# Kernel optimization log

Hardware: AMD Instinct MI355X
Metric: run time of the kernel (lower is better)

The kernel has to match this reference:

```python
import jax, jax.numpy as jnp
import numpy as np

N = 160000          # active voxels / points
C = 128             # embed_channels
K = 27              # 3x3x3 submanifold conv kernel volume
NUM_CLUSTERS = 2048
BN_EPS = 1e-5


def setup_inputs() -> dict:
    key = jax.random.key(0)
    ks = jax.random.split(key, 16)
    s = 0.05
    inp = {
        "feat": jax.random.normal(ks[0], (N, C), jnp.float32),
        "cluster0": jax.random.randint(ks[1], (N,), 0, NUM_CLUSTERS, jnp.int32),
        "cluster1": jax.random.randint(ks[2], (N,), 0, NUM_CLUSTERS, jnp.int32),
        "cluster2": jax.random.randint(ks[3], (N,), 0, NUM_CLUSTERS, jnp.int32),
        "nbr_idx": jax.random.randint(ks[4], (N, K), 0, N, jnp.int32),
        "nbr_mask": jax.random.randint(ks[5], (N, K), 0, 2, jnp.int32) > 0,
        "lw_W": jax.random.normal(ks[6], (3, C, C), jnp.float32) * s,
        "lw_gamma": jnp.ones((3, C), jnp.float32),
        "lw_beta": jnp.zeros((3, C), jnp.float32),
        "w_W": jax.random.normal(ks[7], (3, C, C), jnp.float32) * s,
        "proj_W": jax.random.normal(ks[8], (4, C, C), jnp.float32) * s,
        "proj_gamma": jnp.ones((4, C), jnp.float32),
        "proj_beta": jnp.zeros((4, C), jnp.float32),
        "adaptive_W": jax.random.normal(ks[9], (C, 3), jnp.float32) * s,
        "fuse_W": jax.random.normal(ks[10], (2 * C, C), jnp.float32) * s,
        "fuse_gamma": jnp.ones((C,), jnp.float32),
        "fuse_beta": jnp.zeros((C,), jnp.float32),
        "conv_W": jax.random.normal(ks[11], (2, K, C, C), jnp.float32) * 0.02,
        "conv_gamma": jnp.ones((2, C), jnp.float32),
        "conv_beta": jnp.zeros((2, C), jnp.float32),
    }
    return inp


def _bn(x, gamma, beta):
    # BatchNorm1d, training mode: per-channel stats over points, biased var
    m = jnp.mean(x, axis=0)
    v = jnp.var(x, axis=0)
    return (x - m) * jax.lax.rsqrt(v + BN_EPS) * gamma + beta


def _seg_sum(x, seg):
    return jax.ops.segment_sum(x, seg, num_segments=NUM_CLUSTERS)


def _seg_mean(x, seg):
    s = _seg_sum(x, seg)
    cnt = jax.ops.segment_sum(jnp.ones((x.shape[0], 1), x.dtype), seg,
                              num_segments=NUM_CLUSTERS)
    return s / jnp.maximum(cnt, 1.0)


def _subm_conv(x, W, nbr_idx, nbr_mask):
    # submanifold 3x3x3 conv on active sites: masked gather + per-offset GEMM
    m = nbr_mask.astype(x.dtype)  # [N, K]
    out = jnp.zeros_like(x)
    for k in range(K):
        out = out + (x[nbr_idx[:, k]] * m[:, k:k + 1]) @ W[k]
    return out


def reference(feat, cluster0, cluster1, cluster2, nbr_idx, nbr_mask,
              lw_W, lw_gamma, lw_beta, w_W, proj_W, proj_gamma, proj_beta,
              adaptive_W, fuse_W, fuse_gamma, fuse_beta,
              conv_W, conv_gamma, conv_beta):
    clusters = [cluster0, cluster1, cluster2]
    feats = []
    for i, cl in enumerate(clusters):
        pw = jax.nn.relu(_bn(feat @ lw_W[i], lw_gamma[i], lw_beta[i]))
        pw = pw - _seg_mean(pw, cl)[cl]
        pw = pw @ w_W[i]
        pw = jnp.exp(pw - jnp.max(pw))                      # global max
        pw = pw / (_seg_sum(pw, cl)[cl] + 1e-6)
        pfeat = jax.nn.relu(_bn(feat @ proj_W[i], proj_gamma[i], proj_beta[i])) * pw
        pfeat = _seg_sum(pfeat, cl)[cl]
        feats.append(pfeat)

    adp = jax.nn.softmax(feat @ adaptive_W, axis=1)          # [N, 3]
    feats = jnp.stack(feats, axis=1)                         # [N, 3, C]
    fused_branch = jnp.einsum('ln,lnc->lc', adp, feats)

    f = jax.nn.relu(_bn(feat @ proj_W[3], proj_gamma[3], proj_beta[3]))
    f = jnp.concatenate([f, fused_branch], axis=1)           # [N, 2C]
    f = jax.nn.relu(_bn(f @ fuse_W, fuse_gamma, fuse_beta)) + feat

    res = f
    h = _subm_conv(f, conv_W[0], nbr_idx, nbr_mask)
    h = jax.nn.relu(_bn(h, conv_gamma[0], conv_beta[0]))
    h = _subm_conv(h, conv_W[1], nbr_idx, nbr_mask)
    h = _bn(h, conv_gamma[1], conv_beta[1])
    return jax.nn.relu(h + res)
```

## Files before the change

kernel.cpp:

```cpp
#include <hip/hip_runtime.h>
#include <stdint.h>

#define N_PTS 160000
#define C 128
#define K27 27
#define NCLU 2048
#define BN_EPS 1e-5f
#define KP 136
#define KP2 264

typedef float f32x4 __attribute__((ext_vector_type(4)));
typedef short s16x8 __attribute__((ext_vector_type(8)));

__device__ __forceinline__ float bf2f(unsigned short u){
  union { unsigned int i; float f; } v; v.i = ((unsigned int)u) << 16; return v.f;
}
__device__ __forceinline__ unsigned short f2bf(float f){
  union { float f; unsigned int i; } v; v.f = f;
  unsigned int u = v.i;
  u += 0x7FFFu + ((u >> 16) & 1u);
  return (unsigned short)(u >> 16);
}
__device__ __forceinline__ unsigned int pk(float a, float b){
  return (unsigned int)f2bf(a) | ((unsigned int)f2bf(b) << 16);
}
__device__ __forceinline__ void up2(int w, float& a, float& b){
  a = bf2f((unsigned short)(w & 0xFFFF));
  b = bf2f((unsigned short)(((unsigned int)w) >> 16));
}
__device__ __forceinline__ unsigned int encf(float f){
  union { float f; unsigned int i; } v; v.f = f;
  return ((int)v.i < 0) ? ~v.i : (v.i | 0x80000000u);
}
__device__ __forceinline__ float decf(unsigned int e){
  union { unsigned int i; float f; } v;
  v.i = ((int)e < 0) ? (e ^ 0x80000000u) : ~e;
  return v.f;
}
__device__ __forceinline__ void bn_coef(const float* st, const float* gamma, const float* beta,
                                        int c, float& sc, float& sh){
  float mean = st[c] * (1.0f / N_PTS);
  float var  = st[C + c] * (1.0f / N_PTS) - mean * mean;
  float g = gamma[c] * rsqrtf(fmaxf(var, 0.f) + BN_EPS);
  sc = g; sh = beta[c] - mean * g;
}

__global__ void k_prep_weights(const float* __restrict__ lw, const float* __restrict__ w,
                               const float* __restrict__ proj, const float* __restrict__ conv,
                               const float* __restrict__ fuse,
                               unsigned short* __restrict__ tlw, unsigned short* __restrict__ tw,
                               unsigned short* __restrict__ tproj, unsigned short* __restrict__ tconv,
                               unsigned short* __restrict__ tfuse)
{
  int z = blockIdx.x, tid = threadIdx.x;
  if (z < 64){
    const float* src; unsigned short* dst; bool swz = false;
    if (z < 3){ src = lw + z*16384; dst = tlw + z*16384; }
    else if (z < 6){ src = w + (z-3)*16384; dst = tw + (z-3)*16384; }
    else if (z < 10){ src = proj + (z-6)*16384; dst = tproj + (z-6)*16384; }
    else { src = conv + (z-10)*16384; dst = tconv + (z-10)*16384; swz = true; }
    for (int i = tid; i < 16384; i += 256){
      int n = i >> 7, k = i & 127;
      int pos = swz ? (n*128 + (((k >> 3) ^ (n & 7)) << 3) + (k & 7)) : i;
      dst[pos] = f2bf(src[k*128 + n]);
    }
  } else {
    for (int i = tid; i < 32768; i += 256){
      int n = i >> 8, k = i & 255;
      tfuse[i] = f2bf(fuse[k*128 + n]);
    }
  }
}

__global__ void k_detect_mask(const unsigned int* __restrict__ mw, int* __restrict__ mmode)
{
  __shared__ int flag;
  if (threadIdx.x == 0) flag = 0;
  __syncthreads();
  for (int i = threadIdx.x; i < 4096; i += 256)
    if (mw[i] > 1u) flag = 1;
  __syncthreads();
  if (threadIdx.x == 0) *mmode = flag;
}

__global__ void k_hist(const int* __restrict__ c0, const int* __restrict__ c1,
                       const int* __restrict__ c2, int* __restrict__ hist)
{
  int idx = blockIdx.x*blockDim.x + threadIdx.x;
  int stride = gridDim.x*blockDim.x;
  for (; idx < 3*N_PTS; idx += stride){
    int j = idx / N_PTS, r = idx - j*N_PTS;
    const int* cp = (j==0)?c0:((j==1)?c1:c2);
    atomicAdd(&hist[j*NCLU + cp[r]], 1);
  }
}

__global__ void k_prefix(const int* __restrict__ hist, int* __restrict__ starts,
                         int* __restrict__ cursor)
{
  int j = blockIdx.x, tid = threadIdx.x;
  __shared__ int buf[NCLU];
  __shared__ int csum[256];
  for (int i = tid; i < NCLU; i += 256) buf[i] = hist[j*NCLU + i];
  __syncthreads();
  int s = 0;
  #pragma unroll
  for (int k = 0; k < 8; k++) s += buf[tid*8 + k];
  csum[tid] = s;
  __syncthreads();
  if (tid == 0){
    int run = 0;
    for (int i = 0; i < 256; i++){ int t = csum[i]; csum[i] = run; run += t; }
  }
  __syncthreads();
  int acc = csum[tid];
  #pragma unroll
  for (int k = 0; k < 8; k++){
    int i = tid*8 + k;
    starts[j*(NCLU+1) + i] = acc;
    cursor[j*NCLU + i] = acc;
    acc += buf[i];
  }
  if (tid == 255) starts[j*(NCLU+1) + NCLU] = acc;
}

__global__ void k_scatter(const int* __restrict__ c0, const int* __restrict__ c1,
                          const int* __restrict__ c2, int* __restrict__ cursor,
                          int* __restrict__ perm)
{
  int idx = blockIdx.x*blockDim.x + threadIdx.x;
  int stride = gridDim.x*blockDim.x;
  for (; idx < 3*N_PTS; idx += stride){
    int j = idx / N_PTS, r = idx - j*N_PTS;
    const int* cp = (j==0)?c0:((j==1)?c1:c2);
    int cl = cp[r];
    int slot = atomicAdd(&cursor[j*NCLU + cl], 1);
    perm[j*N_PTS + slot] = r;
  }
}

template<int V>
__global__ void k_seg(const unsigned short* __restrict__ X,
                      const int* __restrict__ perm, const int* __restrict__ starts,
                      const float* __restrict__ st, const float* __restrict__ gamma,
                      const float* __restrict__ beta, float* __restrict__ S)
{
  __shared__ float red[16*128];
  const int cl = blockIdx.x;
  const int p0 = starts[cl], p1 = starts[cl+1];
  const int g = threadIdx.x >> 4, s = threadIdx.x & 15;
  const int c0 = s * 8;
  float sc[8], sh[8];
  #pragma unroll
  for (int j = 0; j < 8; j++) bn_coef(st, gamma, beta, c0 + j, sc[j], sh[j]);
  float acc[8];
  #pragma unroll
  for (int j = 0; j < 8; j++) acc[j] = 0.f;
  for (int p = p0 + g; p < p1; p += 16){
    int row = perm[p];
    int4 v = *(const int4*)(X + (size_t)row*C + c0);
    float f[8];
    up2(v.x, f[0], f[1]); up2(v.y, f[2], f[3]); up2(v.z, f[4], f[5]); up2(v.w, f[6], f[7]);
    #pragma unroll
    for (int j = 0; j < 8; j++) acc[j] += fmaxf(f[j]*sc[j] + sh[j], 0.f);
  }
  #pragma unroll
  for (int j = 0; j < 8; j++) red[g*128 + c0 + j] = acc[j];
  __syncthreads();
  if (threadIdx.x < 128){
    float t = 0.f;
    #pragma unroll
    for (int gg = 0; gg < 16; gg++) t += red[gg*128 + threadIdx.x];
    S[cl*C + threadIdx.x] = t;
  }
}

__global__ void k_seg12(const unsigned short* __restrict__ XP, const unsigned short* __restrict__ X2,
                        const int* __restrict__ perm, const int* __restrict__ starts,
                        const float* __restrict__ st, const float* __restrict__ gamma,
                        const float* __restrict__ beta, const unsigned int* __restrict__ genc,
                        float* __restrict__ S3)
{
  __shared__ float red[16*128];
  const int cl = blockIdx.x;
  const int p0 = starts[cl], p1 = starts[cl+1];
  const int g = threadIdx.x >> 4, s = threadIdx.x & 15;
  const int c0 = s * 8;
  const float gm = decf(*genc);
  float sc[8], sh[8];
  #pragma unroll
  for (int j = 0; j < 8; j++) bn_coef(st, gamma, beta, c0 + j, sc[j], sh[j]);

  float accN[8], accD[8];
  #pragma unroll
  for (int j = 0; j < 8; j++){ accN[j] = 0.f; accD[j] = 0.f; }
  for (int p = p0 + g; p < p1; p += 16){
    int row = perm[p];
    int4 v  = *(const int4*)(XP + (size_t)row*C + c0);
    int4 v2 = *(const int4*)(X2 + (size_t)row*C + c0);
    float f[8], x2[8];
    up2(v.x, f[0], f[1]); up2(v.y, f[2], f[3]); up2(v.z, f[4], f[5]); up2(v.w, f[6], f[7]);
    up2(v2.x, x2[0], x2[1]); up2(v2.y, x2[2], x2[3]); up2(v2.z, x2[4], x2[5]); up2(v2.w, x2[6], x2[7]);
    #pragma unroll
    for (int j = 0; j < 8; j++){
      float e = __expf(x2[j] - gm);
      accD[j] += e;
      accN[j] += fmaxf(f[j]*sc[j] + sh[j], 0.f) * e;
    }
  }
  #pragma unroll
  for (int j = 0; j < 8; j++) red[g*128 + c0 + j] = accN[j];
  __syncthreads();
  float tN = 0.f;
  if (threadIdx.x < 128){
    #pragma unroll
    for (int gg = 0; gg < 16; gg++) tN += red[gg*128 + threadIdx.x];
  }
  __syncthreads();
  #pragma unroll
  for (int j = 0; j < 8; j++) red[g*128 + c0 + j] = accD[j];
  __syncthreads();
  if (threadIdx.x < 128){
    float tD = 0.f;
    #pragma unroll
    for (int gg = 0; gg < 16; gg++) tD += red[gg*128 + threadIdx.x];
    S3[cl*C + threadIdx.x] = tN / (tD + 1e-6f);
  }
}

__global__ void k_adp(const float* __restrict__ feat, const float* __restrict__ aW,
                      float* __restrict__ adp, unsigned short* __restrict__ featb)
{
  __shared__ float wsh[384];
  int tid = threadIdx.x;
  for (int i = tid; i < 384; i += 256) wsh[i] = aW[i];
  __syncthreads();
  int gidx = blockIdx.x*256 + tid;
  int stride = gridDim.x*256;
  for (int t4 = gidx; t4 < N_PTS*4; t4 += stride){
    int row = t4 >> 2, part = t4 & 3;
    float e0=0.f, e1=0.f, e2=0.f;
    const float* fr = feat + (size_t)row*C + part*32;
    unsigned int pb[16];
    #pragma unroll
    for (int c = 0; c < 32; c += 4){
      float4 v = *(const float4*)(fr + c);
      int cc = part*32 + c;
      e0 += v.x*wsh[cc*3+0] + v.y*wsh[(cc+1)*3+0] + v.z*wsh[(cc+2)*3+0] + v.w*wsh[(cc+3)*3+0];
      e1 += v.x*wsh[cc*3+1] + v.y*wsh[(cc+1)*3+1] + v.z*wsh[(cc+2)*3+1] + v.w*wsh[(cc+3)*3+1];
      e2 += v.x*wsh[cc*3+2] + v.y*wsh[(cc+1)*3+2] + v.z*wsh[(cc+2)*3+2] + v.w*wsh[(cc+3)*3+2];
      pb[(c>>1)]   = pk(v.x, v.y);
      pb[(c>>1)+1] = pk(v.z, v.w);
    }
    if (featb){
      int4* dst = (int4*)(featb + (size_t)row*C + part*32);
      dst[0] = make_int4(pb[0], pb[1], pb[2], pb[3]);
      dst[1] = make_int4(pb[4], pb[5], pb[6], pb[7]);
      dst[2] = make_int4(pb[8], pb[9], pb[10], pb[11]);
      dst[3] = make_int4(pb[12], pb[13], pb[14], pb[15]);
    }
    e0 += __shfl_xor(e0, 1); e0 += __shfl_xor(e0, 2);
    e1 += __shfl_xor(e1, 1); e1 += __shfl_xor(e1, 2);
    e2 += __shfl_xor(e2, 1); e2 += __shfl_xor(e2, 2);
    if (part == 0){
      float m = fmaxf(e0, fmaxf(e1, e2));
      float p0 = __expf(e0-m), p1 = __expf(e1-m), p2 = __expf(e2-m);
      float inv = 1.f/(p0+p1+p2);
      adp[row*3+0] = p0*inv; adp[row*3+1] = p1*inv; adp[row*3+2] = p2*inv;
    }
  }
}

__device__ __forceinline__ void gemm_stats_epi(float* csum, float* csq, float* sred,
                                               int wave, int l4, int l16, int tid,
                                               float* __restrict__ stats)
{
  #pragma unroll
  for (int t = 0; t < 8; t++){
    csum[t] += __shfl_xor(csum[t], 16); csum[t] += __shfl_xor(csum[t], 32);
    csq[t]  += __shfl_xor(csq[t], 16);  csq[t]  += __shfl_xor(csq[t], 32);
  }
  if (l4 == 0){
    #pragma unroll
    for (int t = 0; t < 8; t++){
      sred[wave*128 + t*16 + l16] = csum[t];
      sred[512 + wave*128 + t*16 + l16] = csq[t];
    }
  }
  __syncthreads();
  if (tid < 128){
    float s = 0.f, q = 0.f;
    #pragma unroll
    for (int w2 = 0; w2 < 4; w2++){ s += sred[w2*128 + tid]; q += sred[512 + w2*128 + tid]; }
    atomicAdd(&stats[tid], s);
    atomicAdd(&stats[C + tid], q);
  }
}

template<typename AT>
__device__ __forceinline__ void stage_A(const AT* __restrict__ A, unsigned short* As,
                                        int row0, int r, int s)
{
  #pragma unroll
  for (int p = 0; p < 4; p++){
    int rr = r + p * 16;
    if constexpr (sizeof(AT) == 2){
      *(int4*)(As + rr * KP + s * 8) =
        *(const int4*)((const unsigned short*)A + (size_t)(row0 + rr) * C + s * 8);
    } else {
      const float4* ap = (const float4*)((const float*)A + (size_t)(row0 + rr) * C + s * 8);
      float4 x = ap[0], y = ap[1];
      *(int4*)(As + rr * KP + s * 8) =
        make_int4(pk(x.x,x.y), pk(x.z,x.w), pk(y.x,y.y), pk(y.z,y.w));
    }
  }
}

template<typename AT>
__global__ __launch_bounds__(256, 3)
void k_gemm_plain(const AT* __restrict__ A, const unsigned short* __restrict__ Bt,
                  unsigned short* __restrict__ Out, float* __restrict__ stats)
{
  __shared__ unsigned short As[64 * KP];
  __shared__ unsigned short Bs[128 * KP];
  const int tid = threadIdx.x;
  const int row0 = blockIdx.x * 64;
  const int r = tid >> 4, s = tid & 15;
  stage_A<AT>(A, As, row0, r, s);
  #pragma unroll
  for (int p = 0; p < 8; p++){
    int nn = r + p * 16;
    *(int4*)(Bs + nn * KP + s * 8) = *(const int4*)(Bt + nn * C + s * 8);
  }
  __syncthreads();
  const int lane = tid & 63, wave = tid >> 6;
  const int l16 = lane & 15, l4 = lane >> 4, m0 = wave * 16;
  f32x4 acc[8];
  #pragma unroll
  for (int t = 0; t < 8; t++) acc[t] = (f32x4){0.f,0.f,0.f,0.f};
  #pragma unroll
  for (int kk = 0; kk < 4; kk++){
    s16x8 a = *(const s16x8*)(As + (m0 + l16) * KP + kk * 32 + l4 * 8);
    #pragma unroll
    for (int t = 0; t < 8; t++){
      s16x8 b = *(const s16x8*)(Bs + (t * 16 + l16) * KP + kk * 32 + l4 * 8);
      acc[t] = __builtin_amdgcn_mfma_f32_16x16x32_bf16(a, b, acc[t], 0, 0, 0);
    }
  }
  float csum[8], csq[8];
  #pragma unroll
  for (int t = 0; t < 8; t++){
    float ss = 0.f, qq = 0.f;
    #pragma unroll
    for (int q = 0; q < 4; q++){
      float v = acc[t][q];
      int grow = row0 + m0 + l4 * 4 + q;
      Out[(size_t)grow * C + t * 16 + l16] = f2bf(v);
      ss += v; qq += v*v;
    }
    csum[t] = ss; csq[t] = qq;
  }
  __syncthreads();
  gemm_stats_epi(csum, csq, (float*)As, wave, l4, l16, tid, stats);
}

template<typename AT>
__global__ __launch_bounds__(256, 3)
void k_gemm_dual(const AT* __restrict__ A,
                 const unsigned short* __restrict__ Bt0, const unsigned short* __restrict__ Bt1,
                 unsigned short* __restrict__ Out0, unsigned short* __restrict__ Out1,
                 float* __restrict__ stats0, float* __restrict__ stats1)
{
  __shared__ unsigned short As[64 * KP];
  __shared__ unsigned short Bs[128 * KP];
  const int tid = threadIdx.x;
  const int row0 = blockIdx.x * 64;
  const int r = tid >> 4, s = tid & 15;
  const int lane = tid & 63, wave = tid >> 6;
  const int l16 = lane & 15, l4 = lane >> 4, m0 = wave * 16;

  stage_A<AT>(A, As, row0, r, s);
  #pragma unroll
  for (int p = 0; p < 8; p++){
    int nn = r + p * 16;
    *(int4*)(Bs + nn * KP + s * 8) = *(const int4*)(Bt0 + nn * C + s * 8);
  }
  __syncthreads();

  f32x4 acc[8];
  float csum0[8], csq0[8], csum1[8], csq1[8];

  #pragma unroll
  for (int t = 0; t < 8; t++) acc[t] = (f32x4){0.f,0.f,0.f,0.f};
  #pragma unroll
  for (int kk = 0; kk < 4; kk++){
    s16x8 a = *(const s16x8*)(As + (m0 + l16) * KP + kk * 32 + l4 * 8);
    #pragma unroll
    for (int t = 0; t < 8; t++){
      s16x8 b = *(const s16x8*)(Bs + (t * 16 + l16) * KP + kk * 32 + l4 * 8);
      acc[t] = __builtin_amdgcn_mfma_f32_16x16x32_bf16(a, b, acc[t], 0, 0, 0);
    }
  }
  #pragma unroll
  for (int t = 0; t < 8; t++){
    float ss = 0.f, qq = 0.f;
    #pragma unroll
    for (int q = 0; q < 4; q++){
      float v = acc[t][q];
      int grow = row0 + m0 + l4 * 4 + q;
      Out0[(size_t)grow * C + t * 16 + l16] = f2bf(v);
      ss += v; qq += v*v;
    }
    csum0[t] = ss; csq0[t] = qq;
  }
  __syncthreads();
  #pragma unroll
  for (int p = 0; p < 8; p++){
    int nn = r + p * 16;
    *(int4*)(Bs + nn * KP + s * 8) = *(const int4*)(Bt1 + nn * C + s * 8);
  }
  __syncthreads();

  #pragma unroll
  for (int t = 0; t < 8; t++) acc[t] = (f32x4){0.f,0.f,0.f,0.f};
  #pragma unroll
  for (int kk = 0; kk < 4; kk++){
    s16x8 a = *(const s16x8*)(As + (m0 + l16) * KP + kk * 32 + l4 * 8);
    #pragma unroll
    for (int t = 0; t < 8; t++){
      s16x8 b = *(const s16x8*)(Bs + (t * 16 + l16) * KP + kk * 32 + l4 * 8);
      acc[t] = __builtin_amdgcn_mfma_f32_16x16x32_bf16(a, b, acc[t], 0, 0, 0);
    }
  }
  #pragma unroll
  for (int t = 0; t < 8; t++){
    float ss = 0.f, qq = 0.f;
    #pragma unroll
    for (int q = 0; q < 4; q++){
      float v = acc[t][q];
      int grow = row0 + m0 + l4 * 4 + q;
      Out1[(size_t)grow * C + t * 16 + l16] = f2bf(v);
      ss += v; qq += v*v;
    }
    csum1[t] = ss; csq1[t] = qq;
  }
  __syncthreads();
  gemm_stats_epi(csum0, csq0, (float*)As, wave, l4, l16, tid, stats0);
  __syncthreads();
  gemm_stats_epi(csum1, csq1, (float*)As, wave, l4, l16, tid, stats1);
}

__global__ __launch_bounds__(256, 3)
void k_gemm_center(const unsigned short* __restrict__ PW, const unsigned short* __restrict__ Bt,
                   const int* __restrict__ cla, const float* __restrict__ S1,
                   const int* __restrict__ cnt, const float* __restrict__ st,
                   const float* __restrict__ gamma, const float* __restrict__ beta,
                   unsigned short* __restrict__ Out, unsigned int* __restrict__ gmax)
{
  __shared__ unsigned short As[64 * KP];
  __shared__ unsigned short Bs[128 * KP];
  __shared__ float wred[4];
  const int tid = threadIdx.x;
  const int row0 = blockIdx.x * 64;
  const int r = tid >> 4, s = tid & 15;
  float sc[8], sh[8];
  #pragma unroll
  for (int j = 0; j < 8; j++) bn_coef(st, gamma, beta, s*8 + j, sc[j], sh[j]);
  #pragma unroll
  for (int p = 0; p < 4; p++){
    int rr = r + p * 16;
    int grow = row0 + rr;
    int cl = cla[grow];
    float inv = 1.f / fmaxf(1.f, (float)cnt[cl]);
    int4 v = *(const int4*)(PW + (size_t)grow * C + s * 8);
    const float4* mp = (const float4*)(S1 + cl * C + s * 8);
    float4 ma = mp[0], mb = mp[1];
    float f[8];
    up2(v.x, f[0], f[1]); up2(v.y, f[2], f[3]); up2(v.z, f[4], f[5]); up2(v.w, f[6], f[7]);
    float m8[8] = {ma.x,ma.y,ma.z,ma.w,mb.x,mb.y,mb.z,mb.w};
    float o[8];
    #pragma unroll
    for (int j = 0; j < 8; j++) o[j] = fmaxf(f[j]*sc[j] + sh[j], 0.f) - m8[j]*inv;
    *(int4*)(As + rr * KP + s * 8) = make_int4(pk(o[0],o[1]), pk(o[2],o[3]), pk(o[4],o[5]), pk(o[6],o[7]));
  }
  #pragma unroll
  for (int p = 0; p < 8; p++){
    int nn = r + p * 16;
    *(int4*)(Bs + nn * KP + s * 8) = *(const int4*)(Bt + nn * C + s * 8);
  }
  __syncthreads();
  const int lane = tid & 63, wave = tid >> 6;
  const int l16 = lane & 15, l4 = lane >> 4, m0 = wave * 16;
  f32x4 acc[8];
  #pragma unroll
  for (int t = 0; t < 8; t++) acc[t] = (f32x4){0.f,0.f,0.f,0.f};
  #pragma unroll
  for (int kk = 0; kk < 4; kk++){
    s16x8 a = *(const s16x8*)(As + (m0 + l16) * KP + kk * 32 + l4 * 8);
    #pragma unroll
    for (int t = 0; t < 8; t++){
      s16x8 b = *(const s16x8*)(Bs + (t * 16 + l16) * KP + kk * 32 + l4 * 8);
      acc[t] = __builtin_amdgcn_mfma_f32_16x16x32_bf16(a, b, acc[t], 0, 0, 0);
    }
  }
  float mx = -3.4e38f;
  #pragma unroll
  for (int t = 0; t < 8; t++){
    #pragma unroll
    for (int q = 0; q < 4; q++){
      int grow = row0 + m0 + l4 * 4 + q;
      unsigned short ob = f2bf(acc[t][q]);
      Out[(size_t)grow * C + t * 16 + l16] = ob;
      mx = fmaxf(mx, bf2f(ob));
    }
  }
  #pragma unroll
  for (int off = 32; off; off >>= 1) mx = fmaxf(mx, __shfl_xor(mx, off));
  if ((tid & 63) == 0) wred[tid >> 6] = mx;
  __syncthreads();
  if (tid == 0){
    float m = fmaxf(fmaxf(wred[0], wred[1]), fmaxf(wred[2], wred[3]));
    atomicMax(gmax, encf(m));
  }
}

__global__ __launch_bounds__(256, 2)
void k_gemm_fuse(const unsigned short* __restrict__ XP3, const float* __restrict__ adp,
                 const int* __restrict__ cl0, const int* __restrict__ cl1,
                 const int* __restrict__ cl2, const float* __restrict__ S3,
                 const float* __restrict__ st, const float* __restrict__ gamma,
                 const float* __restrict__ beta, const unsigned short* __restrict__ Bt,
                 unsigned short* __restrict__ Out, float* __restrict__ stats)
{
  __shared__ unsigned short As[64 * KP2];
  __shared__ unsigned short Bs[128 * KP];
  __shared__ float scs[C], shs[C];
  const int tid = threadIdx.x;
  if (tid < C){ float a, b; bn_coef(st, gamma, beta, tid, a, b); scs[tid] = a; shs[tid] = b; }
  __syncthreads();
  const int row0 = blockIdx.x * 64;
  const int r8 = tid >> 5, s = tid & 31;
  const int r = tid >> 4, s16i = tid & 15;
  #pragma unroll
  for (int p = 0; p < 8; p++){
    int rr = r8 + p * 8;
    int grow = row0 + rr;
    if (s < 16){
      int c0 = s * 8;
      int4 v = *(const int4*)(XP3 + (size_t)grow * C + c0);
      float f0,f1,f2,f3,f4,f5,f6,f7;
      up2(v.x,f0,f1); up2(v.y,f2,f3); up2(v.z,f4,f5); up2(v.w,f6,f7);
      float o0 = fmaxf(f0*scs[c0+0]+shs[c0+0],0.f), o1 = fmaxf(f1*scs[c0+1]+shs[c0+1],0.f);
      float o2 = fmaxf(f2*scs[c0+2]+shs[c0+2],0.f), o3 = fmaxf(f3*scs[c0+3]+shs[c0+3],0.f);
      float o4 = fmaxf(f4*scs[c0+4]+shs[c0+4],0.f), o5 = fmaxf(f5*scs[c0+5]+shs[c0+5],0.f);
      float o6 = fmaxf(f6*scs[c0+6]+shs[c0+6],0.f), o7 = fmaxf(f7*scs[c0+7]+shs[c0+7],0.f);
      *(int4*)(As + rr * KP2 + c0) = make_int4(pk(o0,o1), pk(o2,o3), pk(o4,o5), pk(o6,o7));
    } else {
      int c0 = (s - 16) * 8;
      float a0 = adp[grow*3+0], a1 = adp[grow*3+1], a2 = adp[grow*3+2];
      const float* p0 = S3 + (size_t)cl0[grow] * C + c0;
      const float* p1 = S3 + (size_t)NCLU * C + (size_t)cl1[grow] * C + c0;
      const float* p2 = S3 + (size_t)2 * NCLU * C + (size_t)cl2[grow] * C + c0;
      float o[8];
      #pragma unroll
      for (int j = 0; j < 8; j++) o[j] = a0*p0[j] + a1*p1[j] + a2*p2[j];
      *(int4*)(As + rr * KP2 + 128 + c0) = make_int4(pk(o[0],o[1]), pk(o[2],o[3]), pk(o[4],o[5]), pk(o[6],o[7]));
    }
  }
  const int lane = tid & 63, wave = tid >> 6;
  const int l16 = lane & 15, l4 = lane >> 4, m0 = wave * 16;
  f32x4 acc[8];
  #pragma unroll
  for (int t = 0; t < 8; t++) acc[t] = (f32x4){0.f,0.f,0.f,0.f};
  #pragma unroll
  for (int h = 0; h < 2; h++){
    if (h) __syncthreads();
    #pragma unroll
    for (int p = 0; p < 8; p++){
      int nn = r + p * 16;
      *(int4*)(Bs + nn * KP + s16i * 8) = *(const int4*)(Bt + nn * 256 + h * 128 + s16i * 8);
    }
    __syncthreads();
    #pragma unroll
    for (int kk = 0; kk < 4; kk++){
      s16x8 a = *(const s16x8*)(As + (m0 + l16) * KP2 + h * 128 + kk * 32 + l4 * 8);
      #pragma unroll
      for (int t = 0; t < 8; t++){
        s16x8 b = *(const s16x8*)(Bs + (t * 16 + l16) * KP + kk * 32 + l4 * 8);
        acc[t] = __builtin_amdgcn_mfma_f32_16x16x32_bf16(a, b, acc[t], 0, 0, 0);
      }
    }
  }
  float csum[8], csq[8];
  #pragma unroll
  for (int t = 0; t < 8; t++){
    float ss = 0.f, qq = 0.f;
    #pragma unroll
    for (int q = 0; q < 4; q++){
      float v = acc[t][q];
      int grow = row0 + m0 + l4 * 4 + q;
      Out[(size_t)grow * C + t * 16 + l16] = f2bf(v);
      ss += v; qq += v*v;
    }
    csum[t] = ss; csq[t] = qq;
  }
  __syncthreads();
  gemm_stats_epi(csum, csq, (float*)As, wave, l4, l16, tid, stats);
}

__device__ __forceinline__ int ld_midx(const int* __restrict__ nbr, const void* __restrict__ maskp,
                                       int mm, int g){
  bool on = mm ? (((const unsigned char*)maskp)[g] != 0)
               : (((const int*)maskp)[g] != 0);
  int v = nbr[g];
  return on ? v : -1;
}

template<typename OT>
__global__ __launch_bounds__(512, 4)
void k_conv(const unsigned short* __restrict__ In, const unsigned short* __restrict__ Wt,
            const int* __restrict__ nbr, const void* __restrict__ maskp,
            const int* __restrict__ mmode, OT* __restrict__ Out, float* __restrict__ stats)
{
  __shared__ unsigned short Bs[2][128*128];
  const int tid = threadIdx.x;
  const int lane = tid & 63, wave = tid >> 6;
  const int l16 = lane & 15, l4 = lane >> 4;
  const int row0 = blockIdx.x * 128;
  const int mm = *mmode;
  const int rg = row0 + wave*16 + l16;
  const s16x8 z8 = (s16x8){0,0,0,0,0,0,0,0};

  auto stage_B = [&](int buf, int k){
    const char* gsrc = (const char*)(Wt + k*16384);
    char* lbase = (char*)&Bs[buf][0];
    #pragma unroll
    for (int p = 0; p < 4; p++){
      int chunk = p*512 + wave*64;
      __builtin_amdgcn_global_load_lds(
        (const unsigned int*)(gsrc + (size_t)(chunk + lane)*16),
        (unsigned int*)(lbase + (size_t)chunk*16), 16, 0, 0);
    }
  };

  f32x4 acc[8];
  #pragma unroll
  for (int t = 0; t < 8; t++) acc[t] = (f32x4){0.f,0.f,0.f,0.f};

  s16x8 A0[4], A1[4];
  auto gather = [&](s16x8* dA, int gi){
    #pragma unroll
    for (int kk = 0; kk < 4; kk++)
      dA[kk] = (gi >= 0) ? *(const s16x8*)(In + (size_t)gi*C + kk*32 + l4*8) : z8;
  };
  auto compute = [&](const s16x8* a, int buf){
    #pragma unroll
    for (int kk = 0; kk < 4; kk++){
      #pragma unroll
      for (int t = 0; t < 8; t++){
        int n = t*16 + l16;
        s16x8 b = *(const s16x8*)(&Bs[buf][n*128 + ((((kk<<2)|l4) ^ (n & 7)) << 3)]);
        acc[t] = __builtin_amdgcn_mfma_f32_16x16x32_bf16(a[kk], b, acc[t], 0, 0, 0);
      }
    }
  };

  stage_B(0, 0);
  int i0 = ld_midx(nbr, maskp, mm, rg*K27 + 0);
  gather(A0, i0);
  i0 = ld_midx(nbr, maskp, mm, rg*K27 + 1);
  __syncthreads();

  #pragma unroll 1
  for (int kb = 0; kb < 13; kb++){
    const int k = kb * 2;
    stage_B(1, k + 1);
    gather(A1, i0);
    i0 = ld_midx(nbr, maskp, mm, rg*K27 + k + 2);
    compute(A0, 0);
    __syncthreads();
    stage_B(0, k + 2);
    gather(A0, i0);
    if (kb < 12) i0 = ld_midx(nbr, maskp, mm, rg*K27 + k + 3);
    compute(A1, 1);
    __syncthreads();
  }
  compute(A0, 0);

  float csum[8], csq[8];
  #pragma unroll
  for (int t = 0; t < 8; t++){
    float ss = 0.f, qq = 0.f;
    #pragma unroll
    for (int q = 0; q < 4; q++){
      float v = acc[t][q];
      int grow = row0 + wave*16 + l4*4 + q;
      if constexpr (sizeof(OT) == 2) Out[(size_t)grow * C + t*16 + l16] = f2bf(v);
      else                           Out[(size_t)grow * C + t*16 + l16] = v;
      ss += v; qq += v*v;
    }
    csum[t] = ss; csq[t] = qq;
  }
  #pragma unroll
  for (int t = 0; t < 8; t++){
    csum[t] += __shfl_xor(csum[t], 16); csum[t] += __shfl_xor(csum[t], 32);
    csq[t]  += __shfl_xor(csq[t], 16);  csq[t]  += __shfl_xor(csq[t], 32);
  }
  __syncthreads();
  float* sred = (float*)Bs;
  if (l4 == 0){
    #pragma unroll
    for (int t = 0; t < 8; t++){
      sred[wave*128 + t*16 + l16] = csum[t];
      sred[1024 + wave*128 + t*16 + l16] = csq[t];
    }
  }
  __syncthreads();
  if (tid < 128){
    float s = 0.f, q = 0.f;
    #pragma unroll
    for (int w2 = 0; w2 < 8; w2++){ s += sred[w2*128 + tid]; q += sred[1024 + w2*128 + tid]; }
    atomicAdd(&stats[tid], s);
    atomicAdd(&stats[C + tid], q);
  }
}

template<int RELU>
__global__ void k_bnapply(const unsigned short* __restrict__ X, unsigned short* __restrict__ Y,
                          const float* __restrict__ st, const float* __restrict__ gamma,
                          const float* __restrict__ beta)
{
  const int total = N_PTS * 16;
  for (int idx = blockIdx.x*blockDim.x + threadIdx.x; idx < total; idx += gridDim.x*blockDim.x){
    int c0 = (idx & 15) * 8;
    int4 v = *(const int4*)(X + (size_t)idx * 8);
    float f[8];
    up2(v.x, f[0], f[1]); up2(v.y, f[2], f[3]); up2(v.z, f[4], f[5]); up2(v.w, f[6], f[7]);
    float o[8];
    #pragma unroll
    for (int j = 0; j < 8; j++){
      float sc, sh; bn_coef(st, gamma, beta, c0 + j, sc, sh);
      float t = f[j] * sc + sh;
      if (RELU) t = fmaxf(t, 0.f);
      o[j] = t;
    }
    *(int4*)(Y + (size_t)idx * 8) = make_int4(pk(o[0],o[1]), pk(o[2],o[3]), pk(o[4],o[5]), pk(o[6],o[7]));
  }
}

__global__ void k_fres(const unsigned short* __restrict__ G, const float* __restrict__ st,
                       const float* __restrict__ gamma, const float* __restrict__ beta,
                       const float* __restrict__ feat, unsigned short* __restrict__ FB)
{
  const int total = N_PTS * 16;
  for (int idx = blockIdx.x*blockDim.x + threadIdx.x; idx < total; idx += gridDim.x*blockDim.x){
    int c0 = (idx & 15) * 8;
    int4 v = *(const int4*)(G + (size_t)idx * 8);
    float f[8];
    up2(v.x, f[0], f[1]); up2(v.y, f[2], f[3]); up2(v.z, f[4], f[5]); up2(v.w, f[6], f[7]);
    const float4* fp = (const float4*)(feat + (size_t)idx * 8);
    float4 fa = fp[0], fb4 = fp[1];
    float fe[8] = {fa.x,fa.y,fa.z,fa.w,fb4.x,fb4.y,fb4.z,fb4.w};
    float o[8];
    #pragma unroll
    for (int j = 0; j < 8; j++){
      float sc, sh; bn_coef(st, gamma, beta, c0 + j, sc, sh);
      o[j] = fmaxf(f[j]*sc + sh, 0.f) + fe[j];
    }
    *(int4*)(FB + (size_t)idx * 8) = make_int4(pk(o[0],o[1]), pk(o[2],o[3]), pk(o[4],o[5]), pk(o[6],o[7]));
  }
}

__global__ void k_final(float* __restrict__ H2, const float* __restrict__ st,
                        const float* __restrict__ gamma, const float* __restrict__ beta,
                        const unsigned short* __restrict__ FB)
{
  const int total = N_PTS * 16;
  for (int idx = blockIdx.x*blockDim.x + threadIdx.x; idx < total; idx += gridDim.x*blockDim.x){
    int c0 = (idx & 15) * 8;
    float4* hp = (float4*)(H2 + (size_t)idx * 8);
    float4 a = hp[0], b = hp[1];
    int4 vf = *(const int4*)(FB + (size_t)idx * 8);
    float fr[8];
    up2(vf.x, fr[0], fr[1]); up2(vf.y, fr[2], fr[3]); up2(vf.z, fr[4], fr[5]); up2(vf.w, fr[6], fr[7]);
    float h[8] = {a.x,a.y,a.z,a.w,b.x,b.y,b.z,b.w};
    #pragma unroll
    for (int j = 0; j < 8; j++){
      float sc, sh; bn_coef(st, gamma, beta, c0 + j, sc, sh);
      h[j] = fmaxf(h[j]*sc + sh + fr[j], 0.f);
    }
    hp[0] = make_float4(h[0],h[1],h[2],h[3]);
    hp[1] = make_float4(h[4],h[5],h[6],h[7]);
  }
}

extern "C" void kernel_launch(void* const* d_in, const int* in_sizes, int n_in,
                              void* d_out, int out_size, void* d_ws, size_t ws_size,
                              hipStream_t stream)
{
  (void)in_sizes; (void)n_in; (void)out_size;
  const float* feat   = (const float*)d_in[0];
  const int* cls[3]   = {(const int*)d_in[1], (const int*)d_in[2], (const int*)d_in[3]};
  const int* nbr      = (const int*)d_in[4];
  const void* mask    = d_in[5];
  const float* lw_W   = (const float*)d_in[6];
  const float* lw_g   = (const float*)d_in[7];
  const float* lw_b   = (const float*)d_in[8];
  const float* w_W    = (const float*)d_in[9];
  const float* proj_W = (const float*)d_in[10];
  const float* proj_g = (const float*)d_in[11];
  const float* proj_b = (const float*)d_in[12];
  const float* adW    = (const float*)d_in[13];
  const float* fuse_W = (const float*)d_in[14];
  const float* fuse_g = (const float*)d_in[15];
  const float* fuse_b = (const float*)d_in[16];
  const float* conv_W = (const float*)d_in[17];
  const float* conv_g = (const float*)d_in[18];
  const float* conv_b = (const float*)d_in[19];

  char* w = (char*)d_ws;
  float*          stats  = (float*)(w + 0);
  unsigned int*   gmax   = (unsigned int*)(w + 10240);
  int*            mmode  = (int*)(w + 10240 + 16);
  int*            hist   = (int*)(w + 10496);
  int*            starts = (int*)(w + 35072);
  int*            cursor = (int*)(w + 59904);
  int*            perm   = (int*)(w + 84480);
  float*          S1     = (float*)(w + 2004480);
  float*          S3     = (float*)(w + 4101632);
  float*          adp    = (float*)(w + 7247360);
  unsigned short* tlw    = (unsigned short*)(w + 9167360);
  unsigned short* tw     = (unsigned short*)(w + 9265664);
  unsigned short* tproj  = (unsigned short*)(w + 9363968);
  unsigned short* tfuse  = (unsigned short*)(w + 9495040);
  unsigned short* tconv  = (unsigned short*)(w + 9560576);
  unsigned short* B1     = (unsigned short*)(w + 11330048);
  unsigned short* B2     = (unsigned short*)(w + 52290048);
  unsigned short* B3     = (unsigned short*)(w + 93250048);
  const bool useb = ws_size >= (size_t)175170048;
  unsigned short* featb = useb ? (unsigned short*)(w + 134210048) : nullptr;

  hipMemsetAsync(d_ws, 0, 35072, stream);

  k_prep_weights<<<65, 256, 0, stream>>>(lw_W, w_W, proj_W, conv_W, fuse_W,
                                         tlw, tw, tproj, tconv, tfuse);
  k_detect_mask<<<1, 256, 0, stream>>>((const unsigned int*)mask, mmode);
  k_hist<<<1024, 256, 0, stream>>>(cls[0], cls[1], cls[2], hist);
  k_prefix<<<3, 256, 0, stream>>>(hist, starts, cursor);
  k_scatter<<<1024, 256, 0, stream>>>(cls[0], cls[1], cls[2], cursor, perm);
  k_adp<<<2500, 256, 0, stream>>>(feat, adW, adp, featb);

  if (useb) k_gemm_plain<unsigned short><<<2500, 256, 0, stream>>>(featb, tlw, B1, stats);
  else      k_gemm_plain<float><<<2500, 256, 0, stream>>>(feat, tlw, B1, stats);

  for (int i = 0; i < 3; i++){
    k_seg<0><<<2048, 256, 0, stream>>>(B1, perm + i*N_PTS, starts + i*(NCLU+1),
                                       stats + i*256, lw_g + i*C, lw_b + i*C, S1);
    k_gemm_center<<<2500, 256, 0, stream>>>(B1, tw + i*16384, cls[i], S1, hist + i*NCLU,
                                            stats + i*256, lw_g + i*C, lw_b + i*C, B3, gmax + i);
    const unsigned short* w0 = tproj + i*16384;
    const unsigned short* w1 = (i < 2) ? (tlw + (i+1)*16384) : (tproj + 3*16384);
    float* st1 = (i < 2) ? (stats + (i+1)*256) : (stats + 6*256);
    if (useb) k_gemm_dual<unsigned short><<<2500, 256, 0, stream>>>(featb, w0, w1, B2, B1,
                                                                    stats + (3+i)*256, st1);
    else      k_gemm_dual<float><<<2500, 256, 0, stream>>>(feat, w0, w1, B2, B1,
                                                           stats + (3+i)*256, st1);
    k_seg12<<<2048, 256, 0, stream>>>(B2, B3, perm + i*N_PTS, starts + i*(NCLU+1),
                                      stats + (3+i)*256, proj_g + i*C, proj_b + i*C,
                                      gmax + i, S3 + (size_t)i*NCLU*C);
  }

  k_gemm_fuse<<<2500, 256, 0, stream>>>(B1, adp, cls[0], cls[1], cls[2], S3,
                                        stats + 6*256, proj_g + 3*C, proj_b + 3*C, tfuse,
                                        B2, stats + 7*256);
  k_fres<<<2048, 256, 0, stream>>>(B2, stats + 7*256, fuse_g, fuse_b, feat, B3);

  k_conv<unsigned short><<<1250, 512, 0, stream>>>(B3, tconv, nbr, mask, mmode, B1, stats + 8*256);
  k_bnapply<1><<<2048, 256, 0, stream>>>(B1, B2, stats + 8*256, conv_g, conv_b);
  k_conv<float><<<1250, 512, 0, stream>>>(B2, tconv + 27*16384, nbr, mask, mmode,
                                          (float*)d_out, stats + 9*256);
  k_final<<<2048, 256, 0, stream>>>((float*)d_out, stats + 9*256, conv_g + C, conv_b + C, B3);
}
```

Baseline: 1.254 ms.

## Switch submanifold conv to 32x32x16 MFMA tiles with 4-wave blocks

```diff
diff --git a/kernel.cpp b/kernel.cpp
--- a/kernel.cpp
+++ b/kernel.cpp
@@ -10,6 +10,7 @@
 #define KP2 264
 
 typedef float f32x4 __attribute__((ext_vector_type(4)));
+typedef float f32x16 __attribute__((ext_vector_type(16)));
 typedef short s16x8 __attribute__((ext_vector_type(8)));
 
 __device__ __forceinline__ float bf2f(unsigned short u){
@@ -617,7 +618,7 @@
 }
 
 template<typename OT>
-__global__ __launch_bounds__(512, 4)
+__global__ __launch_bounds__(256, 2)
 void k_conv(const unsigned short* __restrict__ In, const unsigned short* __restrict__ Wt,
             const int* __restrict__ nbr, const void* __restrict__ maskp,
             const int* __restrict__ mmode, OT* __restrict__ Out, float* __restrict__ stats)
@@ -625,42 +626,43 @@
   __shared__ unsigned short Bs[2][128*128];
   const int tid = threadIdx.x;
   const int lane = tid & 63, wave = tid >> 6;
-  const int l16 = lane & 15, l4 = lane >> 4;
+  const int l31 = lane & 31, half = lane >> 5;
   const int row0 = blockIdx.x * 128;
   const int mm = *mmode;
-  const int rg = row0 + wave*16 + l16;
+  const int rg = row0 + wave*32 + l31;
   const s16x8 z8 = (s16x8){0,0,0,0,0,0,0,0};
 
   auto stage_B = [&](int buf, int k){
     const char* gsrc = (const char*)(Wt + k*16384);
     char* lbase = (char*)&Bs[buf][0];
     #pragma unroll
-    for (int p = 0; p < 4; p++){
-      int chunk = p*512 + wave*64;
+    for (int p = 0; p < 8; p++){
+      int chunk = p*256 + wave*64;
       __builtin_amdgcn_global_load_lds(
         (const unsigned int*)(gsrc + (size_t)(chunk + lane)*16),
         (unsigned int*)(lbase + (size_t)chunk*16), 16, 0, 0);
     }
   };
 
-  f32x4 acc[8];
-  #pragma unroll
-  for (int t = 0; t < 8; t++) acc[t] = (f32x4){0.f,0.f,0.f,0.f};
-
-  s16x8 A0[4], A1[4];
+  f32x16 acc[4];
+  #pragma unroll
+  for (int t = 0; t < 4; t++)
+    acc[t] = (f32x16){0,0,0,0,0,0,0,0,0,0,0,0,0,0,0,0};
+
+  s16x8 A0[8], A1[8];
   auto gather = [&](s16x8* dA, int gi){
     #pragma unroll
-    for (int kk = 0; kk < 4; kk++)
-      dA[kk] = (gi >= 0) ? *(const s16x8*)(In + (size_t)gi*C + kk*32 + l4*8) : z8;
+    for (int s = 0; s < 8; s++)
+      dA[s] = (gi >= 0) ? *(const s16x8*)(In + (size_t)gi*C + s*16 + half*8) : z8;
   };
   auto compute = [&](const s16x8* a, int buf){
     #pragma unroll
-    for (int kk = 0; kk < 4; kk++){
+    for (int s = 0; s < 8; s++){
       #pragma unroll
-      for (int t = 0; t < 8; t++){
-        int n = t*16 + l16;
-        s16x8 b = *(const s16x8*)(&Bs[buf][n*128 + ((((kk<<2)|l4) ^ (n & 7)) << 3)]);
-        acc[t] = __builtin_amdgcn_mfma_f32_16x16x32_bf16(a[kk], b, acc[t], 0, 0, 0);
+      for (int t = 0; t < 4; t++){
+        int n = t*32 + l31;
+        s16x8 b = *(const s16x8*)(&Bs[buf][n*128 + (((s*2 + half) ^ (n & 7)) << 3)]);
+        acc[t] = __builtin_amdgcn_mfma_f32_32x32x16_bf16(a[s], b, acc[t], 0, 0, 0);
       }
     }
   };
@@ -687,39 +689,39 @@
   }
   compute(A0, 0);
 
-  float csum[8], csq[8];
-  #pragma unroll
-  for (int t = 0; t < 8; t++){
+  float csum[4], csq[4];
+  #pragma unroll
+  for (int t = 0; t < 4; t++){
     float ss = 0.f, qq = 0.f;
     #pragma unroll
-    for (int q = 0; q < 4; q++){
-      float v = acc[t][q];
-      int grow = row0 + wave*16 + l4*4 + q;
-      if constexpr (sizeof(OT) == 2) Out[(size_t)grow * C + t*16 + l16] = f2bf(v);
-      else                           Out[(size_t)grow * C + t*16 + l16] = v;
+    for (int r = 0; r < 16; r++){
+      float v = acc[t][r];
+      int grow = row0 + wave*32 + (r & 3) + 8*(r >> 2) + 4*half;
+      if constexpr (sizeof(OT) == 2) Out[(size_t)grow * C + t*32 + l31] = f2bf(v);
+      else                           Out[(size_t)grow * C + t*32 + l31] = v;
       ss += v; qq += v*v;
     }
     csum[t] = ss; csq[t] = qq;
   }
   #pragma unroll
-  for (int t = 0; t < 8; t++){
-    csum[t] += __shfl_xor(csum[t], 16); csum[t] += __shfl_xor(csum[t], 32);
-    csq[t]  += __shfl_xor(csq[t], 16);  csq[t]  += __shfl_xor(csq[t], 32);
+  for (int t = 0; t < 4; t++){
+    csum[t] += __shfl_xor(csum[t], 32);
+    csq[t]  += __shfl_xor(csq[t], 32);
   }
   __syncthreads();
   float* sred = (float*)Bs;
-  if (l4 == 0){
-    #pragma unroll
-    for (int t = 0; t < 8; t++){
-      sred[wave*128 + t*16 + l16] = csum[t];
-      sred[1024 + wave*128 + t*16 + l16] = csq[t];
+  if (half == 0){
+    #pragma unroll
+    for (int t = 0; t < 4; t++){
+      sred[wave*128 + t*32 + l31] = csum[t];
+      sred[512 + wave*128 + t*32 + l31] = csq[t];
     }
   }
   __syncthreads();
   if (tid < 128){
     float s = 0.f, q = 0.f;
     #pragma unroll
-    for (int w2 = 0; w2 < 8; w2++){ s += sred[w2*128 + tid]; q += sred[1024 + w2*128 + tid]; }
+    for (int w2 = 0; w2 < 4; w2++){ s += sred[w2*128 + tid]; q += sred[512 + w2*128 + tid]; }
     atomicAdd(&stats[tid], s);
     atomicAdd(&stats[C + tid], q);
   }
@@ -875,9 +877,9 @@
                                         B2, stats + 7*256);
   k_fres<<<2048, 256, 0, stream>>>(B2, stats + 7*256, fuse_g, fuse_b, feat, B3);
 
-  k_conv<unsigned short><<<1250, 512, 0, stream>>>(B3, tconv, nbr, mask, mmode, B1, stats + 8*256);
+  k_conv<unsigned short><<<1250, 256, 0, stream>>>(B3, tconv, nbr, mask, mmode, B1, stats + 8*256);
   k_bnapply<1><<<2048, 256, 0, stream>>>(B1, B2, stats + 8*256, conv_g, conv_b);
-  k_conv<float><<<1250, 512, 0, stream>>>(B2, tconv + 27*16384, nbr, mask, mmode,
+  k_conv<float><<<1250, 256, 0, stream>>>(B2, tconv + 27*16384, nbr, mask, mmode,
                                           (float*)d_out, stats + 9*256);
   k_final<<<2048, 256, 0, stream>>>((float*)d_out, stats + 9*256, conv_g + C, conv_b + C, B3);
 }
```

New measurement: 1.220 ms. 1.03x faster.
